# Kernel optimization log

Hardware: AMD Instinct MI355X
Metric: run time of the kernel (lower is better)

## Reference

```python
import jax, jax.numpy as jnp
import numpy as np

ALPHA = 1.0  # init alpha


def setup_inputs() -> dict:
    key = jax.random.key(0)
    X = jax.random.normal(key, (4096, 512), dtype=jnp.float32)
    return {"X": X}


def reference(X):
    # Pairwise squared L2 distances via GEMM expansion:
    # ||x_i - x_j||^2 = ||x_i||^2 + ||x_j||^2 - 2 x_i . x_j
    # (same math as ((X[None]-X[:,None])**2).sum(-1) without the O(N^2 D) blow-up)
    sq = jnp.sum(X * X, axis=1)                      # [N]
    d2 = sq[:, None] + sq[None, :] - 2.0 * (X @ X.T)  # [N, N]
    # track_running_stats=True: sigma^2 = alpha * mean(d2), detached in torch
    sigma_square = ALPHA * jax.lax.stop_gradient(jnp.mean(d2))
    return jnp.exp(-d2 / (2.0 * sigma_square))
```

## Files before the change

kernel.cpp:

```cpp
#include <hip/hip_runtime.h>
#include <cstdint>

typedef unsigned short u16;
typedef unsigned int u32;
typedef __bf16 bf16x8 __attribute__((ext_vector_type(8)));
typedef float f32x4 __attribute__((ext_vector_type(4)));

#define N_ROWS 4096
#define D_COLS 512

__device__ __forceinline__ u16 f2bf(float f) {
    u32 u = __float_as_uint(f);
    u += 0x7fffu + ((u >> 16) & 1u);
    return (u16)(u >> 16);
}

#define GLDS(g, l)                                                            \
    __builtin_amdgcn_global_load_lds(                                         \
        (const __attribute__((address_space(1))) void*)(g),                   \
        (__attribute__((address_space(3))) void*)(l), 16, 0, 0)

__global__ __launch_bounds__(256) void k_prep(const float* __restrict__ X,
                                              u16* __restrict__ Xb,
                                              float* __restrict__ sq,
                                              float* __restrict__ partial) {
    __shared__ float cs[4][512];
    const int tid = threadIdx.x;
    const int w = tid >> 6, l = tid & 63;
    const int row0 = blockIdx.x * 16 + w * 4;
    float csum[8] = {0.f,0.f,0.f,0.f,0.f,0.f,0.f,0.f};
#pragma unroll
    for (int r = 0; r < 4; ++r) {
        const int row = row0 + r;
        const float4* src = (const float4*)(X + (size_t)row * D_COLS);
        float4 f0 = src[l * 2];
        float4 f1 = src[l * 2 + 1];
        float v[8] = {f0.x, f0.y, f0.z, f0.w, f1.x, f1.y, f1.z, f1.w};
        float ss = 0.f;
#pragma unroll
        for (int j = 0; j < 8; ++j) { ss += v[j] * v[j]; csum[j] += v[j]; }
        uint4 st;
        st.x = (u32)f2bf(v[0]) | ((u32)f2bf(v[1]) << 16);
        st.y = (u32)f2bf(v[2]) | ((u32)f2bf(v[3]) << 16);
        st.z = (u32)f2bf(v[4]) | ((u32)f2bf(v[5]) << 16);
        st.w = (u32)f2bf(v[6]) | ((u32)f2bf(v[7]) << 16);
        *(uint4*)(Xb + (size_t)row * D_COLS + l * 8) = st;
#pragma unroll
        for (int m = 32; m > 0; m >>= 1) ss += __shfl_xor(ss, m, 64);
        if (l == 0) sq[row] = ss;
    }
#pragma unroll
    for (int j = 0; j < 8; ++j) cs[w][l * 8 + j] = csum[j];
    __syncthreads();
    for (int d = tid; d < 512; d += 256)
        partial[blockIdx.x * 512 + d] = cs[0][d] + cs[1][d] + cs[2][d] + cs[3][d];
}

__global__ __launch_bounds__(256) void k_sigma(const float* __restrict__ sq,
                                               const float* __restrict__ partial,
                                               float* __restrict__ parts) {
    __shared__ float csm[4][64];
    __shared__ float red[8];
    const int g = blockIdx.x;
    const int t = threadIdx.x;
    const int c = g * 64 + (t & 63);
    const int ch = t >> 6;
    float cssum = 0.f;
#pragma unroll 8
    for (int b = ch * 64; b < ch * 64 + 64; ++b) cssum += partial[b * 512 + c];
    csm[ch][t & 63] = cssum;
    float s1 = sq[g * 512 + t] + sq[g * 512 + 256 + t];
    __syncthreads();
    float s2 = 0.f;
    if (t < 64) {
        float v = csm[0][t] + csm[1][t] + csm[2][t] + csm[3][t];
        s2 = v * v;
    }
#pragma unroll
    for (int m = 32; m > 0; m >>= 1) {
        s1 += __shfl_xor(s1, m, 64);
        s2 += __shfl_xor(s2, m, 64);
    }
    if ((t & 63) == 0) { red[ch] = s1; red[4 + ch] = s2; }
    __syncthreads();
    if (t == 0) {
        parts[g] = red[0] + red[1] + red[2] + red[3];
        parts[8 + g] = red[4];
    }
}

__global__ __launch_bounds__(256, 2) void k_gemm(const u16* __restrict__ Xb,
                                                 const float* __restrict__ sq,
                                                 const float* __restrict__ parts,
                                                 float* __restrict__ out) {
    __shared__ __align__(16) u16 As[2][128 * 64];
    __shared__ __align__(16) u16 Bs[2][128 * 64];
    __shared__ float sqA[128], sqB[128];
    __shared__ float c_sh;

    const int tid = threadIdx.x;
    const int lane = tid & 63;
    const int wid = tid >> 6;
    const int wr = wid >> 1, wc = wid & 1;

    const int bid = blockIdx.x;
    const int xcd = bid & 7, rr = bid >> 3;
    const int by = (xcd >> 1) * 8 + (rr & 7);
    const int bx = (xcd & 1) * 16 + (rr >> 3);
    const int i0 = by * 128, j0 = bx * 128;

    const int strow = tid >> 3;
    const int sslot = (tid & 7) ^ (strow & 7);
    const char* xb = (const char*)Xb;
    const char* gA = xb + (size_t)(i0 + strow) * 1024 + sslot * 16;
    const char* gB = xb + (size_t)(j0 + strow) * 1024 + sslot * 16;

#define STAGE(buf, kt)                                                        \
    do {                                                                      \
        _Pragma("unroll")                                                     \
        for (int s = 0; s < 4; ++s) {                                         \
            GLDS(gA + s * 32768 + (kt) * 128,                                 \
                 (char*)As[buf] + s * 4096 + tid * 16);                       \
            GLDS(gB + s * 32768 + (kt) * 128,                                 \
                 (char*)Bs[buf] + s * 4096 + tid * 16);                       \
        }                                                                     \
    } while (0)

    STAGE(0, 0);
    if (tid < 128) sqA[tid] = sq[i0 + tid];
    else           sqB[tid - 128] = sq[j0 + tid - 128];
    if (tid == 0) {
        float S1 = 0.f, S2 = 0.f;
#pragma unroll
        for (int i = 0; i < 8; ++i) { S1 += parts[i]; S2 += parts[8 + i]; }
        const float mean_d2 = 2.f * S1 / (float)N_ROWS
                            - 2.f * S2 / ((float)N_ROWS * (float)N_ROWS);
        c_sh = -1.4426950408889634f / (2.f * mean_d2);
    }

    f32x4 acc[4][4];
#pragma unroll
    for (int m = 0; m < 4; ++m)
#pragma unroll
        for (int n = 0; n < 4; ++n) acc[m][n] = (f32x4){0.f, 0.f, 0.f, 0.f};

    const int frow = lane & 15;
    const int klane = lane >> 4;
    const int s0 = (klane ^ (frow & 7)) << 4;

    for (int kt = 0; kt < 8; ++kt) {
        const int buf = kt & 1;
        __syncthreads();
        if (kt < 7) STAGE(buf ^ 1, kt + 1);
        const char* Ab = (const char*)As[buf];
        const char* Bb = (const char*)Bs[buf];
#pragma unroll
        for (int ks = 0; ks < 2; ++ks) {
            const int kb = s0 ^ (ks << 6);
            bf16x8 a[4], b[4];
#pragma unroll
            for (int i = 0; i < 4; ++i)
                a[i] = *(const bf16x8*)(Ab + (wr * 64 + i * 16 + frow) * 128 + kb);
#pragma unroll
            for (int n = 0; n < 4; ++n)
                b[n] = *(const bf16x8*)(Bb + (wc * 64 + n * 16 + frow) * 128 + kb);
            __builtin_amdgcn_s_setprio(1);
#pragma unroll
            for (int i = 0; i < 4; ++i)
#pragma unroll
                for (int n = 0; n < 4; ++n)
                    acc[i][n] = __builtin_amdgcn_mfma_f32_16x16x32_bf16(
                        a[i], b[n], acc[i][n], 0, 0, 0);
            __builtin_amdgcn_s_setprio(0);
        }
    }
#undef STAGE

    const float cval = c_sh;
    const int q = lane >> 4;
#pragma unroll
    for (int m = 0; m < 4; ++m) {
#pragma unroll
        for (int n = 0; n < 4; ++n) {
            const int col = wc * 64 + n * 16 + frow;
            const float sb = sqB[col];
#pragma unroll
            for (int r = 0; r < 4; ++r) {
                const int row = wr * 64 + m * 16 + q * 4 + r;
                const float d2 = sqA[row] + sb - 2.0f * acc[m][n][r];
                out[(size_t)(i0 + row) * N_ROWS + (j0 + col)] = exp2f(cval * d2);
            }
        }
    }
}

extern "C" void kernel_launch(void* const* d_in, const int* in_sizes, int n_in,
                              void* d_out, int out_size, void* d_ws, size_t ws_size,
                              hipStream_t stream) {
    const float* X = (const float*)d_in[0];
    float* out = (float*)d_out;
    char* ws = (char*)d_ws;

    u16*   Xb   = (u16*)ws;
    float* part = (float*)(ws + (4u << 20));
    float* sq   = (float*)(ws + (4u << 20) + (512u << 10));
    float* prt  = (float*)(ws + (4u << 20) + (512u << 10) + (16u << 10));

    hipLaunchKernelGGL(k_prep, dim3(256), dim3(256), 0, stream, X, Xb, sq, part);
    hipLaunchKernelGGL(k_sigma, dim3(8), dim3(256), 0, stream, sq, part, prt);
    hipLaunchKernelGGL(k_gemm, dim3(1024), dim3(256), 0, stream, Xb, sq, prt, out);
}
```

Measured before the change: 45.99 us.

## Stage GEMM epilogue through LDS for coalesced float4 output stores

The epilogue now writes each 16-row slab of exp results into a padded LDS buffer, which reuses the A/B staging pool. It then reads the slab back so each thread issues coalesced float4 global stores along full rows, replacing the scattered 4-byte stores. It also switches to the hardware exp2 builtin when available. The cost is extra LDS traffic and four additional block barriers per tile.

```diff
diff --git a/kernel.cpp b/kernel.cpp
--- a/kernel.cpp
+++ b/kernel.cpp
@@ -8,6 +8,12 @@
 
 #define N_ROWS 4096
 #define D_COLS 512
+
+#if __has_builtin(__builtin_amdgcn_exp2f)
+#define EXP2(x) __builtin_amdgcn_exp2f(x)
+#else
+#define EXP2(x) exp2f(x)
+#endif
 
 __device__ __forceinline__ u16 f2bf(float f) {
     u32 u = __float_as_uint(f);
@@ -93,8 +99,7 @@
                                                  const float* __restrict__ sq,
                                                  const float* __restrict__ parts,
                                                  float* __restrict__ out) {
-    __shared__ __align__(16) u16 As[2][128 * 64];
-    __shared__ __align__(16) u16 Bs[2][128 * 64];
+    __shared__ __align__(16) char pool[65536];
     __shared__ float sqA[128], sqB[128];
     __shared__ float c_sh;
 
@@ -120,9 +125,9 @@
         _Pragma("unroll")                                                     \
         for (int s = 0; s < 4; ++s) {                                         \
             GLDS(gA + s * 32768 + (kt) * 128,                                 \
-                 (char*)As[buf] + s * 4096 + tid * 16);                       \
+                 pool + (buf) * 16384 + s * 4096 + tid * 16);                 \
             GLDS(gB + s * 32768 + (kt) * 128,                                 \
-                 (char*)Bs[buf] + s * 4096 + tid * 16);                       \
+                 pool + 32768 + (buf) * 16384 + s * 4096 + tid * 16);         \
         }                                                                     \
     } while (0)
 
@@ -146,14 +151,15 @@
 
     const int frow = lane & 15;
     const int klane = lane >> 4;
+    const int q = lane >> 4;
     const int s0 = (klane ^ (frow & 7)) << 4;
 
     for (int kt = 0; kt < 8; ++kt) {
         const int buf = kt & 1;
         __syncthreads();
         if (kt < 7) STAGE(buf ^ 1, kt + 1);
-        const char* Ab = (const char*)As[buf];
-        const char* Bb = (const char*)Bs[buf];
+        const char* Ab = pool + buf * 16384;
+        const char* Bb = pool + 32768 + buf * 16384;
 #pragma unroll
         for (int ks = 0; ks < 2; ++ks) {
             const int kb = s0 ^ (ks << 6);
@@ -176,8 +182,11 @@
     }
 #undef STAGE
 
+    __syncthreads();
+    float (*eps)[132] = (float (*)[132])pool;
     const float cval = c_sh;
-    const int q = lane >> 4;
+    const int lrow = tid >> 3;
+    const int seg = tid & 7;
 #pragma unroll
     for (int m = 0; m < 4; ++m) {
 #pragma unroll
@@ -188,9 +197,19 @@
             for (int r = 0; r < 4; ++r) {
                 const int row = wr * 64 + m * 16 + q * 4 + r;
                 const float d2 = sqA[row] + sb - 2.0f * acc[m][n][r];
-                out[(size_t)(i0 + row) * N_ROWS + (j0 + col)] = exp2f(cval * d2);
+                eps[wr * 16 + q * 4 + r][col] = EXP2(cval * d2);
             }
         }
+        __syncthreads();
+        const int grow = i0 + (lrow >> 4) * 64 + m * 16 + (lrow & 15);
+        float4* orow = (float4*)(out + (size_t)grow * N_ROWS + j0);
+        const float* er = eps[lrow];
+#pragma unroll
+        for (int s = 0; s < 4; ++s) {
+            const int f4 = seg + s * 8;
+            orow[f4] = *(const float4*)(er + f4 * 4);
+        }
+        __syncthreads();
     }
 }
 
```

Measured after the change: 45.93 us. No clear change (-0.1%).
